# Optimization experiments

Measured on AMD Instinct MI355X. Metric: run time of the kernel, lower is better.

Reference implementation:

```python
import jax, jax.numpy as jnp
import numpy as np

H = 16        # GRU hidden / attn embed dim
EPS = 1e-5    # BatchNorm eps


def setup_inputs() -> dict:
    key = jax.random.key(0)
    ks = jax.random.split(key, 24)
    B, T = 32768, 50
    s = 0.1
    inp = {
        "user_id": jax.random.randint(ks[0], (B,), 0, 10000),
        "history_item_id": jax.random.randint(ks[1], (B, T), 0, 10000),
        "history_category_id": jax.random.randint(ks[2], (B, T), 0, 10),
        "target_item_id": jax.random.randint(ks[3], (B, 1), 0, 10000),
        "target_category_id": jax.random.randint(ks[4], (B, 1), 0, 10),
        # embedding tables
        "user_table": jax.random.normal(ks[5], (10000, 16)) * s,
        "item_table": jax.random.normal(ks[6], (10000, 12)) * s,
        "cat_table": jax.random.normal(ks[7], (10, 4)) * s,
        # GRU (torch layout: [3H, in], gates order r,z,n)
        "gru_Wih": jax.random.normal(ks[8], (3 * H, H)) * s,
        "gru_Whh": jax.random.normal(ks[9], (3 * H, H)) * s,
        "gru_bih": jax.random.normal(ks[10], (3 * H,)) * s,
        "gru_bhh": jax.random.normal(ks[11], (3 * H,)) * s,
        # MultiheadAttention, 1 head, embed 16 (in_proj packs q,k,v)
        "mha_Win": jax.random.normal(ks[12], (3 * H, H)) * s,
        "mha_bin": jax.random.normal(ks[13], (3 * H,)) * s,
        "mha_Wout": jax.random.normal(ks[14], (H, H)) * s,
        "mha_bout": jax.random.normal(ks[15], (H,)) * s,
        # BN(48) -> Linear(48,16) -> ReLU -> BN(16) -> Linear(16,2) -> Softmax
        "bn1_g": jnp.ones((48,)),
        "bn1_b": jnp.zeros((48,)),
        "fc1_W": jax.random.normal(ks[16], (16, 48)) * s,
        "fc1_b": jax.random.normal(ks[17], (16,)) * s,
        "bn2_g": jnp.ones((16,)),
        "bn2_b": jnp.zeros((16,)),
        "fc2_W": jax.random.normal(ks[18], (2, 16)) * s,
        "fc2_b": jax.random.normal(ks[19], (2,)) * s,
    }
    return inp


def _gru(x, Wih, Whh, bih, bhh):
    # x: [B, T, H] -> outputs [B, T, H]; torch GRU cell math
    xg = jnp.einsum("bti,gi->btg", x, Wih) + bih           # [B,T,3H]
    xg = jnp.moveaxis(xg, 1, 0)                             # [T,B,3H]
    h0 = jnp.zeros((x.shape[0], H), x.dtype)

    def step(h, xt):
        hg = h @ Whh.T + bhh                                # [B,3H]
        xr, xz, xn = jnp.split(xt, 3, axis=-1)
        hr, hz, hn = jnp.split(hg, 3, axis=-1)
        r = jax.nn.sigmoid(xr + hr)
        z = jax.nn.sigmoid(xz + hz)
        n = jnp.tanh(xn + r * hn)
        h = (1.0 - z) * n + z * h
        return h, h

    _, ys = jax.lax.scan(step, h0, xg)
    return jnp.moveaxis(ys, 0, 1)                           # [B,T,H]


def _mha(q_in, kv_in, Win, bin_, Wout, bout):
    # single-head attention, batch_first
    Wq, Wk, Wv = jnp.split(Win, 3, axis=0)
    bq, bk, bv = jnp.split(bin_, 3, axis=0)
    q = q_in @ Wq.T + bq                                    # [B,T,H]
    k = kv_in @ Wk.T + bk                                   # [B,S,H]
    v = kv_in @ Wv.T + bv                                   # [B,S,H]
    scores = jnp.einsum("btd,bsd->bts", q, k) / jnp.sqrt(jnp.asarray(H, q.dtype))
    attn = jax.nn.softmax(scores, axis=-1)
    ctx = jnp.einsum("bts,bsd->btd", attn, v)
    return ctx @ Wout.T + bout                              # [B,T,H]


def _bn(x, g, b):
    # training-mode BatchNorm1d over batch axis
    mu = x.mean(axis=0)
    var = x.var(axis=0)
    return (x - mu) * jax.lax.rsqrt(var + EPS) * g + b


def reference(user_id, history_item_id, history_category_id, target_item_id,
              target_category_id, user_table, item_table, cat_table,
              gru_Wih, gru_Whh, gru_bih, gru_bhh,
              mha_Win, mha_bin, mha_Wout, mha_bout,
              bn1_g, bn1_b, fc1_W, fc1_b, bn2_g, bn2_b, fc2_W, fc2_b):
    user_emb = user_table[user_id]                          # [B,16]
    hist_emb = jnp.concatenate(
        [item_table[history_item_id], cat_table[history_category_id]], axis=-1)  # [B,T,16]
    tgt_emb = jnp.concatenate(
        [item_table[target_item_id], cat_table[target_category_id]], axis=-1)    # [B,1,16]

    hist_enc = _gru(hist_emb, gru_Wih, gru_Whh, gru_bih, gru_bhh)                 # [B,T,16]
    attn = _mha(hist_enc, tgt_emb, mha_Win, mha_bin, mha_Wout, mha_bout)          # [B,T,16]
    avg = (attn * hist_enc).sum(axis=1)                                           # [B,16]

    all_enc = jnp.concatenate([avg, tgt_emb[:, 0, :], user_emb], axis=1)          # [B,48]
    h = _bn(all_enc, bn1_g, bn1_b)
    h = jax.nn.relu(h @ fc1_W.T + fc1_b)
    h = _bn(h, bn2_g, bn2_b)
    logits = h @ fc2_W.T + fc2_b
    return jax.nn.softmax(logits, axis=-1)                                        # [B,2]
```

## Files before the change

kernel.cpp:

```cpp
#include <hip/hip_runtime.h>

#define BN_EPS 1e-5f

typedef const float* fp;
typedef float f32x4 __attribute__((ext_vector_type(4)));
typedef _Float16 f16x2 __attribute__((ext_vector_type(2)));
typedef _Float16 f16x4 __attribute__((ext_vector_type(4)));
typedef _Float16 f16x8 __attribute__((ext_vector_type(8)));

__device__ __forceinline__ float frcp(float x) { return __builtin_amdgcn_rcpf(x); }
__device__ __forceinline__ float sigm(float x) { return frcp(1.0f + __expf(-x)); }
__device__ __forceinline__ float tanh_fast(float x) { return 1.0f - 2.0f * frcp(1.0f + __expf(2.0f * x)); }

__device__ __forceinline__ f32x4 ld4(const float* p) { return *(const f32x4*)p; }
__device__ __forceinline__ float dot4(f32x4 a, f32x4 b) {
    return a[0] * b[0] + a[1] * b[1] + a[2] * b[2] + a[3] * b[3];
}

#define MFMA32(A, B, C) __builtin_amdgcn_mfma_f32_16x16x32_f16((A), (B), (C), 0, 0, 0)

#define GLDS16(gp, lp) __builtin_amdgcn_global_load_lds( \
    (const __attribute__((address_space(1))) void*)(gp), \
    (__attribute__((address_space(3))) void*)(lp), 16, 0, 0)

__device__ __forceinline__ f16x4 pk_f16(f32x4 v) {
    f16x2 lo = __builtin_bit_cast(f16x2, __builtin_amdgcn_cvt_pkrtz(v[0], v[1]));
    f16x2 hi = __builtin_bit_cast(f16x2, __builtin_amdgcn_cvt_pkrtz(v[2], v[3]));
    return __builtin_shufflevector(lo, hi, 0, 1, 2, 3);
}

__global__ void k_zero(float* __restrict__ stats) { stats[threadIdx.x] = 0.f; }

__device__ __forceinline__ void gru_step_mf(
    f32x4 e4,
    const f16x8& Ar, const f16x8& ArL, const f16x8& Az, const f16x8& AzL,
    const f16x8& Anx, const f16x8& Anh,
    const f32x4& br4, const f32x4& bz4, const f32x4& bxn4, const f32x4& bhn4,
    f32x4& h, f32x4& hsum, f16x4& hh)
{
    f16x4 e_h = pk_f16(e4);
    f16x8 Bhh = __builtin_shufflevector(e_h, hh, 0, 1, 2, 3, 4, 5, 6, 7);
    f16x8 Bee = __builtin_shufflevector(e_h, e_h, 0, 1, 2, 3, 0, 1, 2, 3);
    f16x8 Bh2 = __builtin_shufflevector(hh, hh, 0, 1, 2, 3, 0, 1, 2, 3);
    f32x4 aR = MFMA32(Ar, Bhh, MFMA32(ArL, Bhh, br4));
    f32x4 aZ = MFMA32(Az, Bhh, MFMA32(AzL, Bhh, bz4));
    f32x4 xn = MFMA32(Anx, Bee, bxn4);
    f32x4 hn = MFMA32(Anh, Bh2, bhn4);
    f32x4 r, z, nv;
#pragma unroll
    for (int q = 0; q < 4; ++q) { r[q] = sigm(aR[q]); z[q] = sigm(aZ[q]); }
    f32x4 pre = r * hn + xn;
#pragma unroll
    for (int q = 0; q < 4; ++q) nv[q] = tanh_fast(pre[q]);
    h = z * (h - nv) + nv;
    hsum += h;
    hh = pk_f16(h);
}

__global__ __launch_bounds__(256, 2) void k_gru(
    const int* __restrict__ user_id, const int* __restrict__ hist_item,
    const int* __restrict__ hist_cat, const int* __restrict__ tgt_item,
    const int* __restrict__ tgt_cat,
    fp user_table, fp item_table, fp cat_table,
    fp Whh, fp bhh, fp Wih, fp bih,
    fp mha_Win, fp mha_bin, fp mha_Wout, fp mha_bout,
    float* __restrict__ all_enc, float* __restrict__ stats1, int B, int T)
{
    __shared__ float    s_stage[4][4][256];
    __shared__ unsigned s_ids[4][16 * 67];
    __shared__ float    lds_part[4][96];

    const int tid  = threadIdx.x;
    const int lane = tid & 63;
    const int wid  = tid >> 6;
    const int s    = lane & 15;
    const int hi   = lane >> 4;

    long b = (long)blockIdx.x * 64 + wid * 16 + s;
    const bool act = (b < B);
    if (!act) b = B - 1;

    const int ti  = tgt_item[b];
    const int tc  = tgt_cat[b];
    const int uid = user_id[b];
    asm volatile("" :: "v"(ti), "v"(tc), "v"(uid));

    {
        const int* ip = hist_item + b * T;
        const int* cp = hist_cat  + b * T;
        unsigned* d = &s_ids[wid][s * 67];
        for (int k = hi; k < T; k += 4)
            d[k] = (unsigned)ip[k] | ((unsigned)cp[k] << 16);
    }

    f32x4 wirf = ld4(&Wih[(0  + s) * 16 + 4 * hi]);
    f32x4 wizf = ld4(&Wih[(16 + s) * 16 + 4 * hi]);
    f32x4 winf = ld4(&Wih[(32 + s) * 16 + 4 * hi]);
    f32x4 whrf = ld4(&Whh[(0  + s) * 16 + 4 * hi]);
    f32x4 whzf = ld4(&Whh[(16 + s) * 16 + 4 * hi]);
    f32x4 whnf = ld4(&Whh[(32 + s) * 16 + 4 * hi]);
    f16x4 wir_h = __builtin_convertvector(wirf, f16x4);
    f16x4 wiz_h = __builtin_convertvector(wizf, f16x4);
    f16x4 win_h = __builtin_convertvector(winf, f16x4);
    f16x4 whr_h = __builtin_convertvector(whrf, f16x4);
    f16x4 whz_h = __builtin_convertvector(whzf, f16x4);
    f16x4 whn_h = __builtin_convertvector(whnf, f16x4);
    f16x4 wir_l = __builtin_convertvector(wirf - __builtin_convertvector(wir_h, f32x4), f16x4);
    f16x4 wiz_l = __builtin_convertvector(wizf - __builtin_convertvector(wiz_h, f32x4), f16x4);
    f16x4 win_l = __builtin_convertvector(winf - __builtin_convertvector(win_h, f32x4), f16x4);
    f16x4 whr_l = __builtin_convertvector(whrf - __builtin_convertvector(whr_h, f32x4), f16x4);
    f16x4 whz_l = __builtin_convertvector(whzf - __builtin_convertvector(whz_h, f32x4), f16x4);
    f16x4 whn_l = __builtin_convertvector(whnf - __builtin_convertvector(whn_h, f32x4), f16x4);
    f16x8 Ar  = __builtin_shufflevector(wir_h, whr_h, 0, 1, 2, 3, 4, 5, 6, 7);
    f16x8 ArL = __builtin_shufflevector(wir_l, whr_l, 0, 1, 2, 3, 4, 5, 6, 7);
    f16x8 Az  = __builtin_shufflevector(wiz_h, whz_h, 0, 1, 2, 3, 4, 5, 6, 7);
    f16x8 AzL = __builtin_shufflevector(wiz_l, whz_l, 0, 1, 2, 3, 4, 5, 6, 7);
    f16x8 Anx = __builtin_shufflevector(win_h, win_l, 0, 1, 2, 3, 4, 5, 6, 7);
    f16x8 Anh = __builtin_shufflevector(whn_h, whn_l, 0, 1, 2, 3, 4, 5, 6, 7);
    const f32x4 br4  = ld4(&bih[4 * hi])      + ld4(&bhh[4 * hi]);
    const f32x4 bz4  = ld4(&bih[16 + 4 * hi]) + ld4(&bhh[16 + 4 * hi]);
    const f32x4 bxn4 = ld4(&bih[32 + 4 * hi]);
    const f32x4 bhn4 = ld4(&bhh[32 + 4 * hi]);

    f32x4 h = {0.f, 0.f, 0.f, 0.f}, hsum = {0.f, 0.f, 0.f, 0.f};
    f16x4 hh = {};

    __syncthreads();

    const int T1 = T - 1;
    const unsigned* idsrow = &s_ids[wid][s * 67];
    float* stg = &s_stage[wid][0][0];
    const int l4 = lane * 4;

    const char*   gb   = (hi < 3) ? (const char*)item_table + hi * 16
                                  : (const char*)cat_table;
    const unsigned gsh  = (hi < 3) ? 0u : 16u;
    const unsigned gmul = (hi < 3) ? 48u : 16u;
#define GADDR(pk) (gb + (size_t)(((pk) >> gsh) & 0xffffu) * gmul)

    {
        unsigned p0 = idsrow[0];
        unsigned p1 = idsrow[(1 > T1) ? T1 : 1];
        unsigned p2 = idsrow[(2 > T1) ? T1 : 2];
        unsigned p3 = idsrow[(3 > T1) ? T1 : 3];
        GLDS16(GADDR(p0), stg);
        GLDS16(GADDR(p1), stg + 256);
        GLDS16(GADDR(p2), stg + 512);
        GLDS16(GADDR(p3), stg + 768);
    }
    unsigned idcdA = idsrow[(4 > T1) ? T1 : 4];
    asm volatile("s_waitcnt vmcnt(2)" ::: "memory");
    f32x4 eCur = ld4(stg + l4);

    for (int t = 0; t < T; ++t) {
        asm volatile("s_waitcnt vmcnt(2) lgkmcnt(0)" ::: "memory");
        GLDS16(GADDR(idcdA), stg + ((t & 3) << 8));
        f32x4 eNext = ld4(stg + (((t + 1) & 3) << 8) + l4);
        int t5 = (t + 5 > T1) ? T1 : t + 5;
        unsigned idcdB = idsrow[t5];

        gru_step_mf(eCur, Ar, ArL, Az, AzL, Anx, Anh,
                    br4, bz4, bxn4, bhn4, h, hsum, hh);

        idcdA = idcdB;
        eCur  = eNext;
    }

    const float* itr = item_table + (size_t)ti * 12;
    f32x4 tv0 = ld4(itr), tv1 = ld4(itr + 4), tv2 = ld4(itr + 8);
    f32x4 tv3 = ld4(cat_table + tc * 4);

    f32x4 vq;
#pragma unroll
    for (int q = 0; q < 4; ++q) {
        int row = 32 + 4 * hi + q;
        const float* wv = mha_Win + row * 16;
        vq[q] = mha_bin[row] + dot4(ld4(wv), tv0) + dot4(ld4(wv + 4), tv1)
              + dot4(ld4(wv + 8), tv2) + dot4(ld4(wv + 12), tv3);
    }
    f32x4 vg0, vg1, vg2, vg3;
#pragma unroll
    for (int q = 0; q < 4; ++q) {
        vg0[q] = __shfl_xor(vq[q], (hi ^ 0) << 4);
        vg1[q] = __shfl_xor(vq[q], (hi ^ 1) << 4);
        vg2[q] = __shfl_xor(vq[q], (hi ^ 2) << 4);
        vg3[q] = __shfl_xor(vq[q], (hi ^ 3) << 4);
    }
    f32x4 aj;
#pragma unroll
    for (int q = 0; q < 4; ++q) {
        int row = 4 * hi + q;
        const float* wo = mha_Wout + row * 16;
        aj[q] = mha_bout[row] + dot4(ld4(wo), vg0) + dot4(ld4(wo + 4), vg1)
              + dot4(ld4(wo + 8), vg2) + dot4(ld4(wo + 12), vg3);
    }
    f32x4 avg = aj * hsum;

    f32x4 u4  = ld4(user_table + (size_t)uid * 16 + 4 * hi);
    f32x4 t4v = (hi == 0) ? tv0 : (hi == 1) ? tv1 : (hi == 2) ? tv2 : tv3;

    if (act) {
        float* er = all_enc + b * 48 + 4 * hi;
        *(f32x4*)er        = avg;
        *(f32x4*)(er + 16) = t4v;
        *(f32x4*)(er + 32) = u4;
    }

    const f32x4 zero4 = {0.f, 0.f, 0.f, 0.f};
    f32x4 sa = act ? avg : zero4, st = act ? t4v : zero4, su = act ? u4 : zero4;
    f32x4 qa = sa * sa, qt = st * st, qu = su * su;
#pragma unroll
    for (int m = 1; m <= 8; m <<= 1) {
#pragma unroll
        for (int q = 0; q < 4; ++q) {
            sa[q] += __shfl_xor(sa[q], m);
            st[q] += __shfl_xor(st[q], m);
            su[q] += __shfl_xor(su[q], m);
            qa[q] += __shfl_xor(qa[q], m);
            qt[q] += __shfl_xor(qt[q], m);
            qu[q] += __shfl_xor(qu[q], m);
        }
    }
    if (s == 0) {
        int c = 4 * hi;
#pragma unroll
        for (int q = 0; q < 4; ++q) {
            lds_part[wid][c + q]      = sa[q];
            lds_part[wid][16 + c + q] = st[q];
            lds_part[wid][32 + c + q] = su[q];
            lds_part[wid][48 + c + q] = qa[q];
            lds_part[wid][64 + c + q] = qt[q];
            lds_part[wid][80 + c + q] = qu[q];
        }
    }
    __syncthreads();
    if (tid < 96) {
        float v = lds_part[0][tid] + lds_part[1][tid] + lds_part[2][tid] + lds_part[3][tid];
        atomicAdd(&stats1[tid], v);
    }
}

__global__ __launch_bounds__(256) void k_fc1(
    const float* __restrict__ all_enc, const float* __restrict__ stats,
    fp fc1_W, fp fc1_b, fp g1, fp b1,
    float* __restrict__ hbuf, float* __restrict__ stats2, int B)
{
    const int tid = threadIdx.x, lane = tid & 63, wid = tid >> 6;
    const int j = lane & 15, sl = lane >> 4;
    __shared__ float kk[48], mm[48];
    __shared__ float part[4][32];

    if (tid < 48) {
        float mu  = stats[tid] / (float)B;
        float var = stats[48 + tid] / (float)B - mu * mu;
        float k   = rsqrtf(var + BN_EPS);
        float gk  = g1[tid] * k;
        kk[tid] = gk;
        mm[tid] = b1[tid] - mu * gk;
    }
    __syncthreads();

    float w[48];
    float bj = fc1_b[j];
#pragma unroll
    for (int q = 0; q < 12; ++q) {
        float4 v = *(const float4*)&fc1_W[j * 48 + q * 4];
        w[q * 4 + 0] = v.x * kk[q * 4 + 0];
        w[q * 4 + 1] = v.y * kk[q * 4 + 1];
        w[q * 4 + 2] = v.z * kk[q * 4 + 2];
        w[q * 4 + 3] = v.w * kk[q * 4 + 3];
        bj += v.x * mm[q * 4 + 0] + v.y * mm[q * 4 + 1]
            + v.z * mm[q * 4 + 2] + v.w * mm[q * 4 + 3];
    }

    float sh = 0.f, sq = 0.f;
    for (long b = (long)blockIdx.x * 16 + wid * 4 + sl; b < B; b += (long)gridDim.x * 16) {
        const float* x = all_enc + b * 48;
        float acc = bj;
#pragma unroll
        for (int q = 0; q < 12; ++q) {
            float4 v = *(const float4*)&x[q * 4];
            acc += w[q * 4] * v.x + w[q * 4 + 1] * v.y + w[q * 4 + 2] * v.z + w[q * 4 + 3] * v.w;
        }
        float h = fmaxf(acc, 0.f);
        hbuf[b * 16 + j] = h;
        sh += h; sq += h * h;
    }
    sh += __shfl_xor(sh, 16); sh += __shfl_xor(sh, 32);
    sq += __shfl_xor(sq, 16); sq += __shfl_xor(sq, 32);
    if (sl == 0) { part[wid][j] = sh; part[wid][16 + j] = sq; }
    __syncthreads();
    if (tid < 32) {
        float v = part[0][tid] + part[1][tid] + part[2][tid] + part[3][tid];
        atomicAdd(&stats2[tid], v);
    }
}

__global__ __launch_bounds__(256) void k_out(
    const float* __restrict__ hbuf, const float* __restrict__ stats2,
    fp fc2_W, fp fc2_b, fp g2, fp b2, float* __restrict__ out, int B)
{
    __shared__ float w[34];
    const int tid = threadIdx.x;
    if (tid < 32) {
        int c = tid & 15;
        float mu  = stats2[c] / (float)B;
        float var = stats2[16 + c] / (float)B - mu * mu;
        float gk  = g2[c] * rsqrtf(var + BN_EPS);
        w[tid] = fc2_W[tid] * gk;
    }
    if (tid < 2) {
        float acc = fc2_b[tid];
        for (int c = 0; c < 16; ++c) {
            float mu  = stats2[c] / (float)B;
            float var = stats2[16 + c] / (float)B - mu * mu;
            float gk  = g2[c] * rsqrtf(var + BN_EPS);
            acc += fc2_W[tid * 16 + c] * (b2[c] - mu * gk);
        }
        w[32 + tid] = acc;
    }
    __syncthreads();
    for (long b = (long)blockIdx.x * blockDim.x + threadIdx.x; b < B;
         b += (long)gridDim.x * blockDim.x) {
        const float* h = hbuf + b * 16;
        float l0 = w[32], l1 = w[33];
#pragma unroll
        for (int q = 0; q < 4; ++q) {
            float4 v = *(const float4*)&h[q * 4];
            l0 += w[q * 4] * v.x + w[q * 4 + 1] * v.y + w[q * 4 + 2] * v.z + w[q * 4 + 3] * v.w;
            l1 += w[16 + q * 4] * v.x + w[17 + q * 4] * v.y + w[18 + q * 4] * v.z + w[19 + q * 4] * v.w;
        }
        float m  = fmaxf(l0, l1);
        float e0 = __expf(l0 - m), e1 = __expf(l1 - m);
        float inv = frcp(e0 + e1);
        float2 p; p.x = e0 * inv; p.y = e1 * inv;
        *(float2*)&out[b * 2] = p;
    }
}

extern "C" void kernel_launch(void* const* d_in, const int* in_sizes, int n_in,
                              void* d_out, int out_size, void* d_ws, size_t ws_size,
                              hipStream_t stream)
{
    const int* user_id   = (const int*)d_in[0];
    const int* hist_item = (const int*)d_in[1];
    const int* hist_cat  = (const int*)d_in[2];
    const int* tgt_item  = (const int*)d_in[3];
    const int* tgt_cat   = (const int*)d_in[4];
    fp user_table = (fp)d_in[5];
    fp item_table = (fp)d_in[6];
    fp cat_table  = (fp)d_in[7];
    fp Wih = (fp)d_in[8],  Whh = (fp)d_in[9];
    fp bih = (fp)d_in[10], bhh = (fp)d_in[11];
    fp Win = (fp)d_in[12], binp = (fp)d_in[13];
    fp Wout = (fp)d_in[14], bout = (fp)d_in[15];
    fp g1 = (fp)d_in[16], b1 = (fp)d_in[17];
    fp fc1W = (fp)d_in[18], fc1b = (fp)d_in[19];
    fp g2 = (fp)d_in[20], b2 = (fp)d_in[21];
    fp fc2W = (fp)d_in[22], fc2b = (fp)d_in[23];

    const int B = in_sizes[0];
    const int T = in_sizes[1] / B;

    float* ws       = (float*)d_ws;
    float* stats1   = ws;
    float* stats2   = ws + 96;
    float* all_enc  = ws + 128;
    float* hbuf     = all_enc + (size_t)B * 48;

    hipLaunchKernelGGL(k_zero, dim3(1), dim3(128), 0, stream, ws);

    hipLaunchKernelGGL(k_gru, dim3((B + 63) / 64), dim3(256), 0, stream,
                       user_id, hist_item, hist_cat, tgt_item, tgt_cat,
                       user_table, item_table, cat_table, Whh, bhh, Wih, bih,
                       Win, binp, Wout, bout, all_enc, stats1, B, T);

    hipLaunchKernelGGL(k_fc1, dim3(512), dim3(256), 0, stream,
                       all_enc, stats1, fc1W, fc1b, g1, b1, hbuf, stats2, B);

    hipLaunchKernelGGL(k_out, dim3((B + 255) / 256), dim3(256), 0, stream,
                       hbuf, stats2, fc2W, fc2b, g2, b2, (float*)d_out, B);
}
```

Measured before the change: 66.18 us.

## Process two independent GRU sequences per wave to interleave recurrent chains

Each wavefront now carries two groups of 16 batch rows, running two independent GRU recurrences side by side. The MFMA and transcendental work of the two chains is interleaved so each can hide the other's latency on the serial time dependency. The gather staging buffers and id tables are doubled, and the block count is halved. Launch bounds drop to one block per SIMD pair, so occupancy falls while each wave has more instruction-level parallelism.

```diff
diff --git a/kernel.cpp b/kernel.cpp
--- a/kernel.cpp
+++ b/kernel.cpp
@@ -31,33 +31,91 @@
 
 __global__ void k_zero(float* __restrict__ stats) { stats[threadIdx.x] = 0.f; }
 
-__device__ __forceinline__ void gru_step_mf(
-    f32x4 e4,
+__device__ __forceinline__ void gru_step2(
+    f32x4 e0, f32x4 e1,
     const f16x8& Ar, const f16x8& ArL, const f16x8& Az, const f16x8& AzL,
     const f16x8& Anx, const f16x8& Anh,
     const f32x4& br4, const f32x4& bz4, const f32x4& bxn4, const f32x4& bhn4,
-    f32x4& h, f32x4& hsum, f16x4& hh)
-{
-    f16x4 e_h = pk_f16(e4);
-    f16x8 Bhh = __builtin_shufflevector(e_h, hh, 0, 1, 2, 3, 4, 5, 6, 7);
-    f16x8 Bee = __builtin_shufflevector(e_h, e_h, 0, 1, 2, 3, 0, 1, 2, 3);
-    f16x8 Bh2 = __builtin_shufflevector(hh, hh, 0, 1, 2, 3, 0, 1, 2, 3);
-    f32x4 aR = MFMA32(Ar, Bhh, MFMA32(ArL, Bhh, br4));
-    f32x4 aZ = MFMA32(Az, Bhh, MFMA32(AzL, Bhh, bz4));
-    f32x4 xn = MFMA32(Anx, Bee, bxn4);
-    f32x4 hn = MFMA32(Anh, Bh2, bhn4);
-    f32x4 r, z, nv;
-#pragma unroll
-    for (int q = 0; q < 4; ++q) { r[q] = sigm(aR[q]); z[q] = sigm(aZ[q]); }
-    f32x4 pre = r * hn + xn;
-#pragma unroll
-    for (int q = 0; q < 4; ++q) nv[q] = tanh_fast(pre[q]);
-    h = z * (h - nv) + nv;
-    hsum += h;
-    hh = pk_f16(h);
-}
-
-__global__ __launch_bounds__(256, 2) void k_gru(
+    f32x4& h0, f32x4& hs0, f16x4& hh0,
+    f32x4& h1, f32x4& hs1, f16x4& hh1)
+{
+    f16x4 eh0 = pk_f16(e0);
+    f16x4 eh1 = pk_f16(e1);
+    f16x8 Bhh0 = __builtin_shufflevector(eh0, hh0, 0, 1, 2, 3, 4, 5, 6, 7);
+    f16x8 Bhh1 = __builtin_shufflevector(eh1, hh1, 0, 1, 2, 3, 4, 5, 6, 7);
+    f16x8 Bee0 = __builtin_shufflevector(eh0, eh0, 0, 1, 2, 3, 0, 1, 2, 3);
+    f16x8 Bee1 = __builtin_shufflevector(eh1, eh1, 0, 1, 2, 3, 0, 1, 2, 3);
+    f16x8 Bh20 = __builtin_shufflevector(hh0, hh0, 0, 1, 2, 3, 0, 1, 2, 3);
+    f16x8 Bh21 = __builtin_shufflevector(hh1, hh1, 0, 1, 2, 3, 0, 1, 2, 3);
+    f32x4 aR0 = MFMA32(Ar, Bhh0, MFMA32(ArL, Bhh0, br4));
+    f32x4 aR1 = MFMA32(Ar, Bhh1, MFMA32(ArL, Bhh1, br4));
+    f32x4 aZ0 = MFMA32(Az, Bhh0, MFMA32(AzL, Bhh0, bz4));
+    f32x4 aZ1 = MFMA32(Az, Bhh1, MFMA32(AzL, Bhh1, bz4));
+    f32x4 xn0 = MFMA32(Anx, Bee0, bxn4);
+    f32x4 xn1 = MFMA32(Anx, Bee1, bxn4);
+    f32x4 hn0 = MFMA32(Anh, Bh20, bhn4);
+    f32x4 hn1 = MFMA32(Anh, Bh21, bhn4);
+    f32x4 r0, r1, z0, z1, nv0, nv1;
+#pragma unroll
+    for (int q = 0; q < 4; ++q) {
+        r0[q] = sigm(aR0[q]); r1[q] = sigm(aR1[q]);
+        z0[q] = sigm(aZ0[q]); z1[q] = sigm(aZ1[q]);
+    }
+    f32x4 pre0 = r0 * hn0 + xn0;
+    f32x4 pre1 = r1 * hn1 + xn1;
+#pragma unroll
+    for (int q = 0; q < 4; ++q) {
+        nv0[q] = tanh_fast(pre0[q]);
+        nv1[q] = tanh_fast(pre1[q]);
+    }
+    h0 = z0 * (h0 - nv0) + nv0;
+    h1 = z1 * (h1 - nv1) + nv1;
+    hs0 += h0;
+    hs1 += h1;
+    hh0 = pk_f16(h0);
+    hh1 = pk_f16(h1);
+}
+
+__device__ __forceinline__ void epi_chain(
+    int ti, int tc, int uid, int hi, f32x4 hsum,
+    fp item_table, fp cat_table, fp user_table,
+    fp mha_Win, fp mha_bin, fp mha_Wout, fp mha_bout,
+    f32x4& avg_o, f32x4& t4_o, f32x4& u4_o)
+{
+    const float* itr = item_table + (size_t)ti * 12;
+    f32x4 tv0 = ld4(itr), tv1 = ld4(itr + 4), tv2 = ld4(itr + 8);
+    f32x4 tv3 = ld4(cat_table + tc * 4);
+
+    f32x4 vq;
+#pragma unroll
+    for (int q = 0; q < 4; ++q) {
+        int row = 32 + 4 * hi + q;
+        const float* wv = mha_Win + row * 16;
+        vq[q] = mha_bin[row] + dot4(ld4(wv), tv0) + dot4(ld4(wv + 4), tv1)
+              + dot4(ld4(wv + 8), tv2) + dot4(ld4(wv + 12), tv3);
+    }
+    f32x4 vg0, vg1, vg2, vg3;
+#pragma unroll
+    for (int q = 0; q < 4; ++q) {
+        vg0[q] = __shfl_xor(vq[q], (hi ^ 0) << 4);
+        vg1[q] = __shfl_xor(vq[q], (hi ^ 1) << 4);
+        vg2[q] = __shfl_xor(vq[q], (hi ^ 2) << 4);
+        vg3[q] = __shfl_xor(vq[q], (hi ^ 3) << 4);
+    }
+    f32x4 aj;
+#pragma unroll
+    for (int q = 0; q < 4; ++q) {
+        int row = 4 * hi + q;
+        const float* wo = mha_Wout + row * 16;
+        aj[q] = mha_bout[row] + dot4(ld4(wo), vg0) + dot4(ld4(wo + 4), vg1)
+              + dot4(ld4(wo + 8), vg2) + dot4(ld4(wo + 12), vg3);
+    }
+    avg_o = aj * hsum;
+    u4_o  = ld4(user_table + (size_t)uid * 16 + 4 * hi);
+    t4_o  = (hi == 0) ? tv0 : (hi == 1) ? tv1 : (hi == 2) ? tv2 : tv3;
+}
+
+__global__ __launch_bounds__(256, 1) void k_gru(
     const int* __restrict__ user_id, const int* __restrict__ hist_item,
     const int* __restrict__ hist_cat, const int* __restrict__ tgt_item,
     const int* __restrict__ tgt_cat,
@@ -66,8 +124,8 @@
     fp mha_Win, fp mha_bin, fp mha_Wout, fp mha_bout,
     float* __restrict__ all_enc, float* __restrict__ stats1, int B, int T)
 {
-    __shared__ float    s_stage[4][4][256];
-    __shared__ unsigned s_ids[4][16 * 67];
+    __shared__ float    s_stage[4][2][4][256];
+    __shared__ unsigned s_ids[4][32 * 53];
     __shared__ float    lds_part[4][96];
 
     const int tid  = threadIdx.x;
@@ -76,21 +134,27 @@
     const int s    = lane & 15;
     const int hi   = lane >> 4;
 
-    long b = (long)blockIdx.x * 64 + wid * 16 + s;
-    const bool act = (b < B);
-    if (!act) b = B - 1;
-
-    const int ti  = tgt_item[b];
-    const int tc  = tgt_cat[b];
-    const int uid = user_id[b];
-    asm volatile("" :: "v"(ti), "v"(tc), "v"(uid));
+    long b0 = (long)blockIdx.x * 128 + wid * 32 + s;
+    long b1 = b0 + 16;
+    const bool act0 = (b0 < B), act1 = (b1 < B);
+    if (!act0) b0 = B - 1;
+    if (!act1) b1 = B - 1;
+
+    const int ti0 = tgt_item[b0], tc0 = tgt_cat[b0], uid0 = user_id[b0];
+    const int ti1 = tgt_item[b1], tc1 = tgt_cat[b1], uid1 = user_id[b1];
+    asm volatile("" :: "v"(ti0), "v"(tc0), "v"(uid0), "v"(ti1), "v"(tc1), "v"(uid1));
 
     {
-        const int* ip = hist_item + b * T;
-        const int* cp = hist_cat  + b * T;
-        unsigned* d = &s_ids[wid][s * 67];
-        for (int k = hi; k < T; k += 4)
-            d[k] = (unsigned)ip[k] | ((unsigned)cp[k] << 16);
+        const int* ip0 = hist_item + b0 * T;
+        const int* cp0 = hist_cat  + b0 * T;
+        const int* ip1 = hist_item + b1 * T;
+        const int* cp1 = hist_cat  + b1 * T;
+        unsigned* d0 = &s_ids[wid][s * 53];
+        unsigned* d1 = &s_ids[wid][(16 + s) * 53];
+        for (int k = hi; k < T; k += 4) {
+            d0[k] = (unsigned)ip0[k] | ((unsigned)cp0[k] << 16);
+            d1[k] = (unsigned)ip1[k] | ((unsigned)cp1[k] << 16);
+        }
     }
 
     f32x4 wirf = ld4(&Wih[(0  + s) * 16 + 4 * hi]);
@@ -122,14 +186,17 @@
     const f32x4 bxn4 = ld4(&bih[32 + 4 * hi]);
     const f32x4 bhn4 = ld4(&bhh[32 + 4 * hi]);
 
-    f32x4 h = {0.f, 0.f, 0.f, 0.f}, hsum = {0.f, 0.f, 0.f, 0.f};
-    f16x4 hh = {};
+    f32x4 h0 = {0.f,0.f,0.f,0.f}, hs0 = {0.f,0.f,0.f,0.f};
+    f32x4 h1 = {0.f,0.f,0.f,0.f}, hs1 = {0.f,0.f,0.f,0.f};
+    f16x4 hh0 = {}, hh1 = {};
 
     __syncthreads();
 
     const int T1 = T - 1;
-    const unsigned* idsrow = &s_ids[wid][s * 67];
-    float* stg = &s_stage[wid][0][0];
+    const unsigned* ids0 = &s_ids[wid][s * 53];
+    const unsigned* ids1 = &s_ids[wid][(16 + s) * 53];
+    float* stg0 = &s_stage[wid][0][0][0];
+    float* stg1 = &s_stage[wid][1][0][0];
     const int l4 = lane * 4;
 
     const char*   gb   = (hi < 3) ? (const char*)item_table + hi * 16
@@ -138,77 +205,59 @@
     const unsigned gmul = (hi < 3) ? 48u : 16u;
 #define GADDR(pk) (gb + (size_t)(((pk) >> gsh) & 0xffffu) * gmul)
 
-    {
-        unsigned p0 = idsrow[0];
-        unsigned p1 = idsrow[(1 > T1) ? T1 : 1];
-        unsigned p2 = idsrow[(2 > T1) ? T1 : 2];
-        unsigned p3 = idsrow[(3 > T1) ? T1 : 3];
-        GLDS16(GADDR(p0), stg);
-        GLDS16(GADDR(p1), stg + 256);
-        GLDS16(GADDR(p2), stg + 512);
-        GLDS16(GADDR(p3), stg + 768);
-    }
-    unsigned idcdA = idsrow[(4 > T1) ? T1 : 4];
-    asm volatile("s_waitcnt vmcnt(2)" ::: "memory");
-    f32x4 eCur = ld4(stg + l4);
+#pragma unroll
+    for (int d = 0; d < 4; ++d) {
+        int td = (d > T1) ? T1 : d;
+        unsigned p0 = ids0[td], p1 = ids1[td];
+        GLDS16(GADDR(p0), stg0 + d * 256);
+        GLDS16(GADDR(p1), stg1 + d * 256);
+    }
+    unsigned idA0 = ids0[(4 > T1) ? T1 : 4];
+    unsigned idA1 = ids1[(4 > T1) ? T1 : 4];
+    asm volatile("s_waitcnt vmcnt(6)" ::: "memory");
+    f32x4 eCur0 = ld4(stg0 + l4);
+    f32x4 eCur1 = ld4(stg1 + l4);
 
     for (int t = 0; t < T; ++t) {
-        asm volatile("s_waitcnt vmcnt(2) lgkmcnt(0)" ::: "memory");
-        GLDS16(GADDR(idcdA), stg + ((t & 3) << 8));
-        f32x4 eNext = ld4(stg + (((t + 1) & 3) << 8) + l4);
+        asm volatile("s_waitcnt vmcnt(4) lgkmcnt(0)" ::: "memory");
+        GLDS16(GADDR(idA0), stg0 + ((t & 3) << 8));
+        GLDS16(GADDR(idA1), stg1 + ((t & 3) << 8));
+        f32x4 eN0 = ld4(stg0 + (((t + 1) & 3) << 8) + l4);
+        f32x4 eN1 = ld4(stg1 + (((t + 1) & 3) << 8) + l4);
         int t5 = (t + 5 > T1) ? T1 : t + 5;
-        unsigned idcdB = idsrow[t5];
-
-        gru_step_mf(eCur, Ar, ArL, Az, AzL, Anx, Anh,
-                    br4, bz4, bxn4, bhn4, h, hsum, hh);
-
-        idcdA = idcdB;
-        eCur  = eNext;
-    }
-
-    const float* itr = item_table + (size_t)ti * 12;
-    f32x4 tv0 = ld4(itr), tv1 = ld4(itr + 4), tv2 = ld4(itr + 8);
-    f32x4 tv3 = ld4(cat_table + tc * 4);
-
-    f32x4 vq;
-#pragma unroll
-    for (int q = 0; q < 4; ++q) {
-        int row = 32 + 4 * hi + q;
-        const float* wv = mha_Win + row * 16;
-        vq[q] = mha_bin[row] + dot4(ld4(wv), tv0) + dot4(ld4(wv + 4), tv1)
-              + dot4(ld4(wv + 8), tv2) + dot4(ld4(wv + 12), tv3);
-    }
-    f32x4 vg0, vg1, vg2, vg3;
-#pragma unroll
-    for (int q = 0; q < 4; ++q) {
-        vg0[q] = __shfl_xor(vq[q], (hi ^ 0) << 4);
-        vg1[q] = __shfl_xor(vq[q], (hi ^ 1) << 4);
-        vg2[q] = __shfl_xor(vq[q], (hi ^ 2) << 4);
-        vg3[q] = __shfl_xor(vq[q], (hi ^ 3) << 4);
-    }
-    f32x4 aj;
-#pragma unroll
-    for (int q = 0; q < 4; ++q) {
-        int row = 4 * hi + q;
-        const float* wo = mha_Wout + row * 16;
-        aj[q] = mha_bout[row] + dot4(ld4(wo), vg0) + dot4(ld4(wo + 4), vg1)
-              + dot4(ld4(wo + 8), vg2) + dot4(ld4(wo + 12), vg3);
-    }
-    f32x4 avg = aj * hsum;
-
-    f32x4 u4  = ld4(user_table + (size_t)uid * 16 + 4 * hi);
-    f32x4 t4v = (hi == 0) ? tv0 : (hi == 1) ? tv1 : (hi == 2) ? tv2 : tv3;
-
-    if (act) {
-        float* er = all_enc + b * 48 + 4 * hi;
-        *(f32x4*)er        = avg;
-        *(f32x4*)(er + 16) = t4v;
-        *(f32x4*)(er + 32) = u4;
+        unsigned idB0 = ids0[t5], idB1 = ids1[t5];
+
+        gru_step2(eCur0, eCur1, Ar, ArL, Az, AzL, Anx, Anh,
+                  br4, bz4, bxn4, bhn4, h0, hs0, hh0, h1, hs1, hh1);
+
+        idA0 = idB0; idA1 = idB1;
+        eCur0 = eN0; eCur1 = eN1;
+    }
+
+    f32x4 avg0, t40, u40, avg1, t41, u41;
+    epi_chain(ti0, tc0, uid0, hi, hs0, item_table, cat_table, user_table,
+              mha_Win, mha_bin, mha_Wout, mha_bout, avg0, t40, u40);
+    epi_chain(ti1, tc1, uid1, hi, hs1, item_table, cat_table, user_table,
+              mha_Win, mha_bin, mha_Wout, mha_bout, avg1, t41, u41);
+
+    if (act0) {
+        float* er = all_enc + b0 * 48 + 4 * hi;
+        *(f32x4*)er        = avg0;
+        *(f32x4*)(er + 16) = t40;
+        *(f32x4*)(er + 32) = u40;
+    }
+    if (act1) {
+        float* er = all_enc + b1 * 48 + 4 * hi;
+        *(f32x4*)er        = avg1;
+        *(f32x4*)(er + 16) = t41;
+        *(f32x4*)(er + 32) = u41;
     }
 
     const f32x4 zero4 = {0.f, 0.f, 0.f, 0.f};
-    f32x4 sa = act ? avg : zero4, st = act ? t4v : zero4, su = act ? u4 : zero4;
-    f32x4 qa = sa * sa, qt = st * st, qu = su * su;
+    f32x4 a0 = act0 ? avg0 : zero4, t0v = act0 ? t40 : zero4, u0v = act0 ? u40 : zero4;
+    f32x4 a1 = act1 ? avg1 : zero4, t1v = act1 ? t41 : zero4, u1v = act1 ? u41 : zero4;
+    f32x4 sa = a0 + a1, st = t0v + t1v, su = u0v + u1v;
+    f32x4 qa = a0 * a0 + a1 * a1, qt = t0v * t0v + t1v * t1v, qu = u0v * u0v + u1v * u1v;
 #pragma unroll
     for (int m = 1; m <= 8; m <<= 1) {
 #pragma unroll
@@ -370,7 +419,7 @@
 
     hipLaunchKernelGGL(k_zero, dim3(1), dim3(128), 0, stream, ws);
 
-    hipLaunchKernelGGL(k_gru, dim3((B + 63) / 64), dim3(256), 0, stream,
+    hipLaunchKernelGGL(k_gru, dim3((B + 127) / 128), dim3(256), 0, stream,
                        user_id, hist_item, hist_cat, tgt_item, tgt_cat,
                        user_table, item_table, cat_table, Whh, bhh, Wih, bih,
                        Win, binp, Wout, bout, all_enc, stats1, B, T);
```

New measurement: 71.42 us. 7.9% more time.

## Deepen GRU embedding prefetch to 8 slots and batch four steps per iteration

Applied to the files above, without the earlier changes.

The GRU staging ring grows from 4 to 8 slots. The time loop is unrolled by 4, so each iteration issues four global-to-LDS embedding loads and reads its ids with vector loads; the id rows are padded to 64 entries, each row is clamped to the last valid step, and the row stride moves to 68. The intent is to amortise waitcnt stalls and keep more gathers in flight behind the MFMA recurrence. The zeroing kernel is replaced by hipMemsetAsync, and the fc1 grid doubles. The cost is more LDS per block, which may lower occupancy, and extra id loads when T is less than 64.

```diff
diff --git a/kernel.cpp b/kernel.cpp
--- a/kernel.cpp
+++ b/kernel.cpp
@@ -7,6 +7,7 @@
 typedef _Float16 f16x2 __attribute__((ext_vector_type(2)));
 typedef _Float16 f16x4 __attribute__((ext_vector_type(4)));
 typedef _Float16 f16x8 __attribute__((ext_vector_type(8)));
+typedef unsigned u32x4 __attribute__((ext_vector_type(4)));
 
 __device__ __forceinline__ float frcp(float x) { return __builtin_amdgcn_rcpf(x); }
 __device__ __forceinline__ float sigm(float x) { return frcp(1.0f + __expf(-x)); }
@@ -28,8 +29,6 @@
     f16x2 hi = __builtin_bit_cast(f16x2, __builtin_amdgcn_cvt_pkrtz(v[2], v[3]));
     return __builtin_shufflevector(lo, hi, 0, 1, 2, 3);
 }
-
-__global__ void k_zero(float* __restrict__ stats) { stats[threadIdx.x] = 0.f; }
 
 __device__ __forceinline__ void gru_step_mf(
     f32x4 e4,
@@ -66,8 +65,8 @@
     fp mha_Win, fp mha_bin, fp mha_Wout, fp mha_bout,
     float* __restrict__ all_enc, float* __restrict__ stats1, int B, int T)
 {
-    __shared__ float    s_stage[4][4][256];
-    __shared__ unsigned s_ids[4][16 * 67];
+    __shared__ float    s_stage[4][8][256];
+    __shared__ unsigned s_ids[4][16 * 68];
     __shared__ float    lds_part[4][96];
 
     const int tid  = threadIdx.x;
@@ -85,12 +84,16 @@
     const int uid = user_id[b];
     asm volatile("" :: "v"(ti), "v"(tc), "v"(uid));
 
+    const int T1 = T - 1;
+
     {
         const int* ip = hist_item + b * T;
         const int* cp = hist_cat  + b * T;
-        unsigned* d = &s_ids[wid][s * 67];
-        for (int k = hi; k < T; k += 4)
-            d[k] = (unsigned)ip[k] | ((unsigned)cp[k] << 16);
+        unsigned* d = &s_ids[wid][s * 68];
+        for (int k = hi; k < 64; k += 4) {
+            int src = (k <= T1) ? k : T1;
+            d[k] = (unsigned)ip[src] | ((unsigned)cp[src] << 16);
+        }
     }
 
     f32x4 wirf = ld4(&Wih[(0  + s) * 16 + 4 * hi]);
@@ -127,8 +130,7 @@
 
     __syncthreads();
 
-    const int T1 = T - 1;
-    const unsigned* idsrow = &s_ids[wid][s * 67];
+    const unsigned* idsrow = &s_ids[wid][s * 68];
     float* stg = &s_stage[wid][0][0];
     const int l4 = lane * 4;
 
@@ -139,31 +141,49 @@
 #define GADDR(pk) (gb + (size_t)(((pk) >> gsh) & 0xffffu) * gmul)
 
     {
-        unsigned p0 = idsrow[0];
-        unsigned p1 = idsrow[(1 > T1) ? T1 : 1];
-        unsigned p2 = idsrow[(2 > T1) ? T1 : 2];
-        unsigned p3 = idsrow[(3 > T1) ? T1 : 3];
-        GLDS16(GADDR(p0), stg);
-        GLDS16(GADDR(p1), stg + 256);
-        GLDS16(GADDR(p2), stg + 512);
-        GLDS16(GADDR(p3), stg + 768);
-    }
-    unsigned idcdA = idsrow[(4 > T1) ? T1 : 4];
-    asm volatile("s_waitcnt vmcnt(2)" ::: "memory");
-    f32x4 eCur = ld4(stg + l4);
-
-    for (int t = 0; t < T; ++t) {
-        asm volatile("s_waitcnt vmcnt(2) lgkmcnt(0)" ::: "memory");
-        GLDS16(GADDR(idcdA), stg + ((t & 3) << 8));
-        f32x4 eNext = ld4(stg + (((t + 1) & 3) << 8) + l4);
-        int t5 = (t + 5 > T1) ? T1 : t + 5;
-        unsigned idcdB = idsrow[t5];
-
-        gru_step_mf(eCur, Ar, ArL, Az, AzL, Anx, Anh,
-                    br4, bz4, bxn4, bhn4, h, hsum, hh);
-
-        idcdA = idcdB;
-        eCur  = eNext;
+        u32x4 i03 = *(const u32x4*)&idsrow[0];
+        u32x4 i47 = *(const u32x4*)&idsrow[4];
+        GLDS16(GADDR(i03[0]), stg);
+        GLDS16(GADDR(i03[1]), stg + 256);
+        GLDS16(GADDR(i03[2]), stg + 512);
+        GLDS16(GADDR(i03[3]), stg + 768);
+        GLDS16(GADDR(i47[0]), stg + 1024);
+        GLDS16(GADDR(i47[1]), stg + 1280);
+        GLDS16(GADDR(i47[2]), stg + 1536);
+        GLDS16(GADDR(i47[3]), stg + 1792);
+    }
+    u32x4 idn = *(const u32x4*)&idsrow[8];
+
+    const int M    = T >> 2;
+    const int tail = T & 3;
+
+    for (int k = 0; k < M; ++k) {
+        const int base = k << 2;
+        asm volatile("s_waitcnt vmcnt(4)" ::: "memory");
+        f32x4 e0 = ld4(stg + (((base + 0) & 7) << 8) + l4);
+        f32x4 e1 = ld4(stg + (((base + 1) & 7) << 8) + l4);
+        f32x4 e2 = ld4(stg + (((base + 2) & 7) << 8) + l4);
+        f32x4 e3 = ld4(stg + (((base + 3) & 7) << 8) + l4);
+        u32x4 idc = idn;
+        idn = *(const u32x4*)&idsrow[base + 12];
+
+        gru_step_mf(e0, Ar, ArL, Az, AzL, Anx, Anh, br4, bz4, bxn4, bhn4, h, hsum, hh);
+        gru_step_mf(e1, Ar, ArL, Az, AzL, Anx, Anh, br4, bz4, bxn4, bhn4, h, hsum, hh);
+        gru_step_mf(e2, Ar, ArL, Az, AzL, Anx, Anh, br4, bz4, bxn4, bhn4, h, hsum, hh);
+        gru_step_mf(e3, Ar, ArL, Az, AzL, Anx, Anh, br4, bz4, bxn4, bhn4, h, hsum, hh);
+
+        asm volatile("s_waitcnt lgkmcnt(0)" ::: "memory");
+        GLDS16(GADDR(idc[0]), stg + (((base + 0) & 7) << 8));
+        GLDS16(GADDR(idc[1]), stg + (((base + 1) & 7) << 8));
+        GLDS16(GADDR(idc[2]), stg + (((base + 2) & 7) << 8));
+        GLDS16(GADDR(idc[3]), stg + (((base + 3) & 7) << 8));
+    }
+    if (tail) {
+        asm volatile("s_waitcnt vmcnt(0)" ::: "memory");
+        for (int t = M << 2; t < T; ++t) {
+            f32x4 e = ld4(stg + ((t & 7) << 8) + l4);
+            gru_step_mf(e, Ar, ArL, Az, AzL, Anx, Anh, br4, bz4, bxn4, bhn4, h, hsum, hh);
+        }
     }
 
     const float* itr = item_table + (size_t)ti * 12;
@@ -368,14 +388,14 @@
     float* all_enc  = ws + 128;
     float* hbuf     = all_enc + (size_t)B * 48;
 
-    hipLaunchKernelGGL(k_zero, dim3(1), dim3(128), 0, stream, ws);
+    hipMemsetAsync(ws, 0, 128 * sizeof(float), stream);
 
     hipLaunchKernelGGL(k_gru, dim3((B + 63) / 64), dim3(256), 0, stream,
                        user_id, hist_item, hist_cat, tgt_item, tgt_cat,
                        user_table, item_table, cat_table, Whh, bhh, Wih, bih,
                        Win, binp, Wout, bout, all_enc, stats1, B, T);
 
-    hipLaunchKernelGGL(k_fc1, dim3(512), dim3(256), 0, stream,
+    hipLaunchKernelGGL(k_fc1, dim3(1024), dim3(256), 0, stream,
                        all_enc, stats1, fc1W, fc1b, g1, b1, hbuf, stats2, B);
 
     hipLaunchKernelGGL(k_out, dim3((B + 255) / 256), dim3(256), 0, stream,
```

Result: slower. 70.84 us (+7.0%).
